# Optimization experiments

Measured on AMD Instinct MI355X. Metric: run time of the kernel, lower is better.

Reference implementation:

```python
import jax, jax.numpy as jnp
import numpy as np

B, D, L, G, K, U, OUT = 131072, 256, 3, 4, 128, 64, 10


def setup_inputs() -> dict:
    key = jax.random.key(0)
    k1, k2, k3, k4 = jax.random.split(key, 4)
    x = jax.random.normal(k1, (B, D), dtype=jnp.float32)
    # per-level, per-group input node coords into the previous level's output
    idx = jax.random.randint(k2, (L, G, K), 0, D, dtype=jnp.int32)
    # per-group kernels [fan_in, units] and biases [units], stacked
    W = jax.random.normal(k3, (L, G, K, U), dtype=jnp.float32) * 0.1
    b = jnp.zeros((L, G, U), dtype=jnp.float32)
    W_out = jax.random.normal(k4, (D, OUT), dtype=jnp.float32) * 0.1
    b_out = jnp.zeros((OUT,), dtype=jnp.float32)
    return {"x": x, "idx": idx, "W": W, "b": b, "W_out": W_out, "b_out": b_out}


def reference(x, idx, W, b, W_out, b_out):
    # Each topological level: for every dependency-group g, gather K scalar
    # columns from the previous level (the per-node slice+concat in the
    # original), tiny matmul [B,K]@[K,U] + bias, tanh; level output is the
    # concat of group outputs -> [B, G*U]. Groups share shapes, so they are
    # batched over axis g with a single einsum per level.
    h = x
    n_levels = W.shape[0]
    for l in range(n_levels):  # small fixed loop over topology levels
        gathered = h[:, idx[l]]                                  # [B, G, K]
        z = jnp.einsum('bgk,gku->bgu', gathered, W[l]) + b[l]    # [B, G, U]
        h = jnp.tanh(z).reshape(z.shape[0], -1)                  # [B, G*U]
    # output level: single group fed by all previous nodes, linear out activation
    return h @ W_out + b_out                                      # [B, OUT]
```

## Files before the change

### kernel.cpp

```cpp
#include <hip/hip_runtime.h>

typedef unsigned short ushort_t;
typedef __attribute__((ext_vector_type(8))) short short8;
typedef __attribute__((ext_vector_type(4))) float floatx4;
typedef __attribute__((ext_vector_type(4))) unsigned short ushort4v;

#define DD 256
#define LL 3
#define GG 4
#define KK 128
#define UU 64
#define OUTN 10
#define HSTRIDE 264

__device__ __forceinline__ ushort_t f2bf(float f) {
  unsigned u = __builtin_bit_cast(unsigned, f);
  u = (u + 0x7FFFu + ((u >> 16) & 1u)) >> 16;
  return (ushort_t)u;
}

__device__ __forceinline__ float fast_tanh(float x) {
  float e = __builtin_amdgcn_exp2f(x * 2.885390081777927f);
  return __builtin_fmaf(-2.0f, __builtin_amdgcn_rcpf(e + 1.0f), 1.0f);
}

__global__ __launch_bounds__(256) void prep_kernel(
    const int* __restrict__ idx, const float* __restrict__ W,
    const float* __restrict__ Wout, ushort_t* __restrict__ AT,
    ushort_t* __restrict__ WoT) {
  int b = blockIdx.x;
  int t = threadIdx.x;
  if (b < LL * DD) {
    int l = b >> 8, n = b & 255, g = n >> 6, u = n & 63;
    __shared__ int sidx[KK];
    __shared__ float sw[KK];
    if (t < KK) {
      sidx[t] = idx[(l * GG + g) * KK + t];
      sw[t]   = W[((size_t)((l * GG + g) * KK + t)) * UU + u];
    }
    __syncthreads();
    float s = 0.f;
#pragma unroll 8
    for (int j = 0; j < KK; j++) s += (sidx[j] == t) ? sw[j] : 0.f;
    AT[(b << 8) | t] = f2bf(s);
  } else {
    int e2 = (b - LL * DD) * 256 + t;
    int n = e2 >> 8, k = e2 & 255;
    WoT[e2] = (n < OUTN) ? f2bf(Wout[k * OUTN + n]) : (ushort_t)0;
  }
}

__global__ __launch_bounds__(256) void fused_kernel(
    const float* __restrict__ x, const float* __restrict__ bias,
    const float* __restrict__ bout, const ushort_t* __restrict__ AT,
    const ushort_t* __restrict__ WoT, float* __restrict__ out) {
  __shared__ ushort_t hbuf[64 * HSTRIDE];

  const int tid  = threadIdx.x;
  const int wave = tid >> 6;
  const int lane = tid & 63;
  const int quad = lane >> 4;
  const int l16  = lane & 15;
  const long row0 = (long)blockIdx.x * 64;

  const float4* xv = (const float4*)(x + row0 * DD);
#pragma unroll
  for (int i = 0; i < 16; i++) {
    int f  = tid + i * 256;
    int r  = f >> 6;
    int c4 = f & 63;
    float4 v = xv[r * 64 + c4];
    ushort4v uv;
    uv.x = f2bf(v.x); uv.y = f2bf(v.y); uv.z = f2bf(v.z); uv.w = f2bf(v.w);
    *(ushort4v*)&hbuf[r * HSTRIDE + c4 * 4] = uv;
  }
  __syncthreads();

  const floatx4 zero = {0.f, 0.f, 0.f, 0.f};

#pragma unroll
  for (int l = 0; l < 3; l++) {
    const ushort_t* A = AT + l * (DD * DD);

    short8 wf[4][8];
#pragma unroll
    for (int nt = 0; nt < 4; nt++)
#pragma unroll
      for (int ks = 0; ks < 8; ks++)
        wf[nt][ks] = *(const short8*)&A[(wave * 64 + nt * 16 + l16) * 256 + ks * 32 + quad * 8];

    floatx4 acc[4][4];
#pragma unroll
    for (int mt = 0; mt < 4; mt++)
#pragma unroll
      for (int nt = 0; nt < 4; nt++) acc[mt][nt] = zero;

#pragma unroll
    for (int ks = 0; ks < 8; ks++) {
      const int kb = ks * 32 + quad * 8;
      short8 bf[4];
#pragma unroll
      for (int mt = 0; mt < 4; mt++)
        bf[mt] = *(const short8*)&hbuf[(mt * 16 + l16) * HSTRIDE + kb];
#pragma unroll
      for (int mt = 0; mt < 4; mt++)
#pragma unroll
        for (int nt = 0; nt < 4; nt++)
          acc[mt][nt] = __builtin_amdgcn_mfma_f32_16x16x32_bf16(wf[nt][ks], bf[mt], acc[mt][nt], 0, 0, 0);
    }
    __syncthreads();

#pragma unroll
    for (int nt = 0; nt < 4; nt++) {
      float4 bv = *(const float4*)&bias[(l * GG + wave) * UU + nt * 16 + quad * 4];
#pragma unroll
      for (int mt = 0; mt < 4; mt++) {
        ushort4v hv;
        hv.x = f2bf(fast_tanh(acc[mt][nt][0] + bv.x));
        hv.y = f2bf(fast_tanh(acc[mt][nt][1] + bv.y));
        hv.z = f2bf(fast_tanh(acc[mt][nt][2] + bv.z));
        hv.w = f2bf(fast_tanh(acc[mt][nt][3] + bv.w));
        *(ushort4v*)&hbuf[(mt * 16 + l16) * HSTRIDE + wave * 64 + nt * 16 + quad * 4] = hv;
      }
    }
    __syncthreads();
  }

  short8 wof[8];
#pragma unroll
  for (int ks = 0; ks < 8; ks++)
    wof[ks] = *(const short8*)&WoT[l16 * 256 + ks * 32 + quad * 8];

  floatx4 accf = zero;
#pragma unroll
  for (int ks = 0; ks < 8; ks++) {
    short8 bf = *(const short8*)&hbuf[(wave * 16 + l16) * HSTRIDE + ks * 32 + quad * 8];
    accf = __builtin_amdgcn_mfma_f32_16x16x32_bf16(wof[ks], bf, accf, 0, 0, 0);
  }

  const long obase = (row0 + wave * 16 + l16) * OUTN;
  if (quad < 2) {
    float2 p0 = {accf[0] + bout[quad * 4 + 0], accf[1] + bout[quad * 4 + 1]};
    float2 p1 = {accf[2] + bout[quad * 4 + 2], accf[3] + bout[quad * 4 + 3]};
    *(float2*)&out[obase + quad * 4]     = p0;
    *(float2*)&out[obase + quad * 4 + 2] = p1;
  } else if (quad == 2) {
    float2 p0 = {accf[0] + bout[8], accf[1] + bout[9]};
    *(float2*)&out[obase + 8] = p0;
  }
}

extern "C" void kernel_launch(void* const* d_in, const int* in_sizes, int n_in,
                              void* d_out, int out_size, void* d_ws, size_t ws_size,
                              hipStream_t stream) {
  const float* x    = (const float*)d_in[0];
  const int*   idx  = (const int*)d_in[1];
  const float* W    = (const float*)d_in[2];
  const float* b    = (const float*)d_in[3];
  const float* Wout = (const float*)d_in[4];
  const float* bout = (const float*)d_in[5];
  float* out = (float*)d_out;

  ushort_t* AT  = (ushort_t*)d_ws;
  ushort_t* WoT = AT + LL * DD * DD;

  prep_kernel<<<LL * DD + 16, 256, 0, stream>>>(idx, W, Wout, AT, WoT);
  fused_kernel<<<2048, 256, 0, stream>>>(x, b, bout, AT, WoT, out);
}
```

Before: 298.0 us.

## Software-pipeline weight and activation fragment loads across levels and k-steps

Restructures the per-level MFMA loop so weight fragments are streamed two k-steps ahead and LDS activation fragments one k-step ahead, instead of loading all 32 weight fragments up front. The first two k-slices of the next level's weights (or the output weights) are prefetched before the barrier of the current level, and the first level's prefetch is issued before the x staging. Launch bounds now request two blocks per SM to cap register use. The goal is to hide global and LDS latency behind MFMA work, at the cost of more live registers and a possible spill under the new occupancy cap.

Result: faster. 286.5 us (-3.9%).

```diff
diff --git a/kernel.cpp b/kernel.cpp
--- a/kernel.cpp
+++ b/kernel.cpp
@@ -50,7 +50,67 @@
   }
 }
 
-__global__ __launch_bounds__(256) void fused_kernel(
+#define RUN_LEVEL(Ab, PF, BPTR)                                                \
+  {                                                                            \
+    const ushort_t* hsrc = hbuf + l16 * HSTRIDE + quad * 8;                    \
+    short8 wf[8][4];                                                           \
+    _Pragma("unroll") for (int nt = 0; nt < 4; nt++) {                         \
+      wf[0][nt] = pw0[nt];                                                     \
+      wf[1][nt] = pw1[nt];                                                     \
+    }                                                                          \
+    short8 bf[8][4];                                                           \
+    _Pragma("unroll") for (int mt = 0; mt < 4; mt++)                           \
+      bf[0][mt] = *(const short8*)&hsrc[mt * 16 * HSTRIDE];                    \
+    floatx4 acc[4][4];                                                         \
+    _Pragma("unroll") for (int mt = 0; mt < 4; mt++)                           \
+      _Pragma("unroll") for (int nt = 0; nt < 4; nt++) acc[mt][nt] = zero;     \
+    _Pragma("unroll") for (int ks = 0; ks < 8; ks++) {                         \
+      if (ks + 2 < 8) {                                                        \
+        _Pragma("unroll") for (int nt = 0; nt < 4; nt++)                       \
+          wf[ks + 2][nt] = *(const short8*)&(Ab)[nt * 4096 + (ks + 2) * 32];   \
+      }                                                                        \
+      if (ks + 1 < 8) {                                                        \
+        _Pragma("unroll") for (int mt = 0; mt < 4; mt++)                       \
+          bf[ks + 1][mt] =                                                     \
+              *(const short8*)&hsrc[mt * 16 * HSTRIDE + (ks + 1) * 32];        \
+      }                                                                        \
+      _Pragma("unroll") for (int mt = 0; mt < 4; mt++)                         \
+        _Pragma("unroll") for (int nt = 0; nt < 4; nt++)                       \
+          acc[mt][nt] = __builtin_amdgcn_mfma_f32_16x16x32_bf16(               \
+              wf[ks][nt], bf[ks][mt], acc[mt][nt], 0, 0, 0);                   \
+    }                                                                          \
+    PF;                                                                        \
+    __syncthreads();                 \
+    _Pragma("unroll") for (int nt = 0; nt < 4; nt++) {                         \
+      float4 bv = *(const float4*)&(BPTR)[nt * 16 + quad * 4];                 \
+      _Pragma("unroll") for (int mt = 0; mt < 4; mt++) {                       \
+        ushort4v hv;                                                           \
+        hv.x = f2bf(fast_tanh(acc[mt][nt][0] + bv.x));                         \
+        hv.y = f2bf(fast_tanh(acc[mt][nt][1] + bv.y));                         \
+        hv.z = f2bf(fast_tanh(acc[mt][nt][2] + bv.z));                         \
+        hv.w = f2bf(fast_tanh(acc[mt][nt][3] + bv.w));                         \
+        *(ushort4v*)&hbuf[(mt * 16 + l16) * HSTRIDE + wave * 64 + nt * 16 +    \
+                          quad * 4] = hv;                                      \
+      }                                                                        \
+    }                                                                          \
+    __syncthreads();                                                           \
+  }
+
+#define PF_NEXT(Anext)                                                         \
+  {                                                                            \
+    _Pragma("unroll") for (int nt = 0; nt < 4; nt++)                           \
+        pw0[nt] = *(const short8*)&(Anext)[nt * 4096];                         \
+    _Pragma("unroll") for (int nt = 0; nt < 4; nt++)                           \
+        pw1[nt] = *(const short8*)&(Anext)[nt * 4096 + 32];                    \
+  }
+
+#define PF_WOUT                                                                \
+  {                                                                            \
+    _Pragma("unroll") for (int ks = 0; ks < 8; ks++)                           \
+        wof[ks] = *(const short8*)&WoT[l16 * 256 + ks * 32 + quad * 8];        \
+  }
+
+__global__ __launch_bounds__(256, 2) void fused_kernel(
     const float* __restrict__ x, const float* __restrict__ bias,
     const float* __restrict__ bout, const ushort_t* __restrict__ AT,
     const ushort_t* __restrict__ WoT, float* __restrict__ out) {
@@ -62,6 +122,14 @@
   const int quad = lane >> 4;
   const int l16  = lane & 15;
   const long row0 = (long)blockIdx.x * 64;
+  const floatx4 zero = {0.f, 0.f, 0.f, 0.f};
+
+  const ushort_t* A0 = AT + (wave * 64 + l16) * 256 + quad * 8;
+  const ushort_t* A1 = A0 + 65536;
+  const ushort_t* A2 = A0 + 131072;
+
+  short8 pw0[4], pw1[4], wof[8];
+  PF_NEXT(A0);
 
   const float4* xv = (const float4*)(x + row0 * DD);
 #pragma unroll
@@ -76,66 +144,19 @@
   }
   __syncthreads();
 
-  const floatx4 zero = {0.f, 0.f, 0.f, 0.f};
+  const float* b0 = bias + (0 * GG + wave) * UU;
+  const float* b1 = bias + (1 * GG + wave) * UU;
+  const float* b2 = bias + (2 * GG + wave) * UU;
 
-#pragma unroll
-  for (int l = 0; l < 3; l++) {
-    const ushort_t* A = AT + l * (DD * DD);
-
-    short8 wf[4][8];
-#pragma unroll
-    for (int nt = 0; nt < 4; nt++)
-#pragma unroll
-      for (int ks = 0; ks < 8; ks++)
-        wf[nt][ks] = *(const short8*)&A[(wave * 64 + nt * 16 + l16) * 256 + ks * 32 + quad * 8];
-
-    floatx4 acc[4][4];
-#pragma unroll
-    for (int mt = 0; mt < 4; mt++)
-#pragma unroll
-      for (int nt = 0; nt < 4; nt++) acc[mt][nt] = zero;
-
-#pragma unroll
-    for (int ks = 0; ks < 8; ks++) {
-      const int kb = ks * 32 + quad * 8;
-      short8 bf[4];
-#pragma unroll
-      for (int mt = 0; mt < 4; mt++)
-        bf[mt] = *(const short8*)&hbuf[(mt * 16 + l16) * HSTRIDE + kb];
-#pragma unroll
-      for (int mt = 0; mt < 4; mt++)
-#pragma unroll
-        for (int nt = 0; nt < 4; nt++)
-          acc[mt][nt] = __builtin_amdgcn_mfma_f32_16x16x32_bf16(wf[nt][ks], bf[mt], acc[mt][nt], 0, 0, 0);
-    }
-    __syncthreads();
-
-#pragma unroll
-    for (int nt = 0; nt < 4; nt++) {
-      float4 bv = *(const float4*)&bias[(l * GG + wave) * UU + nt * 16 + quad * 4];
-#pragma unroll
-      for (int mt = 0; mt < 4; mt++) {
-        ushort4v hv;
-        hv.x = f2bf(fast_tanh(acc[mt][nt][0] + bv.x));
-        hv.y = f2bf(fast_tanh(acc[mt][nt][1] + bv.y));
-        hv.z = f2bf(fast_tanh(acc[mt][nt][2] + bv.z));
-        hv.w = f2bf(fast_tanh(acc[mt][nt][3] + bv.w));
-        *(ushort4v*)&hbuf[(mt * 16 + l16) * HSTRIDE + wave * 64 + nt * 16 + quad * 4] = hv;
-      }
-    }
-    __syncthreads();
-  }
-
-  short8 wof[8];
-#pragma unroll
-  for (int ks = 0; ks < 8; ks++)
-    wof[ks] = *(const short8*)&WoT[l16 * 256 + ks * 32 + quad * 8];
+  RUN_LEVEL(A0, PF_NEXT(A1), b0);
+  RUN_LEVEL(A1, PF_NEXT(A2), b1);
+  RUN_LEVEL(A2, PF_WOUT,     b2);
 
   floatx4 accf = zero;
 #pragma unroll
   for (int ks = 0; ks < 8; ks++) {
-    short8 bf = *(const short8*)&hbuf[(wave * 16 + l16) * HSTRIDE + ks * 32 + quad * 8];
-    accf = __builtin_amdgcn_mfma_f32_16x16x32_bf16(wof[ks], bf, accf, 0, 0, 0);
+    short8 bfr = *(const short8*)&hbuf[(wave * 16 + l16) * HSTRIDE + ks * 32 + quad * 8];
+    accf = __builtin_amdgcn_mfma_f32_16x16x32_bf16(wof[ks], bfr, accf, 0, 0, 0);
   }
 
   const long obase = (row0 + wave * 16 + l16) * OUTN;
```

## Double rows per block and stream weight fragments with prefetch per k-step

Applied to the files above, without the earlier changes.

Each block now handles 128 rows instead of 64, so every weight fragment loaded from global memory is reused across twice as many MFMA tiles. Instead of preloading all 32 weight fragments per level, the kernel streams them one k-step ahead (double-buffered) to reduce register pressure. The bias is folded into the accumulator initialisation, and bf16 packing uses a perm-based round-half-up instead of round-to-nearest-even. The output stores are widened to float4. The larger shared buffer and launch_bounds(256,2) lower occupancy, trading latency hiding for reuse.

Result: faster. 271.1 us (-9.0%).

```diff
diff --git a/kernel.cpp b/kernel.cpp
--- a/kernel.cpp
+++ b/kernel.cpp
@@ -3,7 +3,6 @@
 typedef unsigned short ushort_t;
 typedef __attribute__((ext_vector_type(8))) short short8;
 typedef __attribute__((ext_vector_type(4))) float floatx4;
-typedef __attribute__((ext_vector_type(4))) unsigned short ushort4v;
 
 #define DD 256
 #define LL 3
@@ -12,11 +11,18 @@
 #define UU 64
 #define OUTN 10
 #define HSTRIDE 264
+#define MROWS 128
 
 __device__ __forceinline__ ushort_t f2bf(float f) {
   unsigned u = __builtin_bit_cast(unsigned, f);
   u = (u + 0x7FFFu + ((u >> 16) & 1u)) >> 16;
   return (ushort_t)u;
+}
+
+__device__ __forceinline__ unsigned pack_bf2(float lo, float hi) {
+  unsigned a = __builtin_bit_cast(unsigned, hi) + 0x8000u;
+  unsigned b = __builtin_bit_cast(unsigned, lo) + 0x8000u;
+  return __builtin_amdgcn_perm(a, b, 0x07060302u);
 }
 
 __device__ __forceinline__ float fast_tanh(float x) {
@@ -50,77 +56,80 @@
   }
 }
 
-__global__ __launch_bounds__(256) void fused_kernel(
+__global__ __launch_bounds__(256, 2) void fused_kernel(
     const float* __restrict__ x, const float* __restrict__ bias,
     const float* __restrict__ bout, const ushort_t* __restrict__ AT,
     const ushort_t* __restrict__ WoT, float* __restrict__ out) {
-  __shared__ ushort_t hbuf[64 * HSTRIDE];
+  __shared__ ushort_t hbuf[MROWS * HSTRIDE];
 
   const int tid  = threadIdx.x;
   const int wave = tid >> 6;
   const int lane = tid & 63;
   const int quad = lane >> 4;
   const int l16  = lane & 15;
-  const long row0 = (long)blockIdx.x * 64;
+  const long row0 = (long)blockIdx.x * MROWS;
 
   const float4* xv = (const float4*)(x + row0 * DD);
 #pragma unroll
-  for (int i = 0; i < 16; i++) {
+  for (int i = 0; i < 32; i++) {
     int f  = tid + i * 256;
     int r  = f >> 6;
     int c4 = f & 63;
     float4 v = xv[r * 64 + c4];
-    ushort4v uv;
-    uv.x = f2bf(v.x); uv.y = f2bf(v.y); uv.z = f2bf(v.z); uv.w = f2bf(v.w);
-    *(ushort4v*)&hbuf[r * HSTRIDE + c4 * 4] = uv;
+    uint2 w;
+    w.x = pack_bf2(v.x, v.y);
+    w.y = pack_bf2(v.z, v.w);
+    *(uint2*)&hbuf[r * HSTRIDE + c4 * 4] = w;
   }
   __syncthreads();
 
-  const floatx4 zero = {0.f, 0.f, 0.f, 0.f};
+#pragma unroll 1
+  for (int l = 0; l < 3; l++) {
+    const ushort_t* Ab = AT + l * (DD * DD) + (wave * UU + l16) * DD + quad * 8;
+    const ushort_t* hsrc = hbuf + l16 * HSTRIDE + quad * 8;
 
+    floatx4 acc[8][4];
 #pragma unroll
-  for (int l = 0; l < 3; l++) {
-    const ushort_t* A = AT + l * (DD * DD);
+    for (int nt = 0; nt < 4; nt++) {
+      float4 bv = *(const float4*)&bias[(l * GG + wave) * UU + nt * 16 + quad * 4];
+      floatx4 ini = {bv.x, bv.y, bv.z, bv.w};
+#pragma unroll
+      for (int mt = 0; mt < 8; mt++) acc[mt][nt] = ini;
+    }
 
-    short8 wf[4][8];
+    short8 wf[4], wfn[4];
 #pragma unroll
-    for (int nt = 0; nt < 4; nt++)
-#pragma unroll
-      for (int ks = 0; ks < 8; ks++)
-        wf[nt][ks] = *(const short8*)&A[(wave * 64 + nt * 16 + l16) * 256 + ks * 32 + quad * 8];
-
-    floatx4 acc[4][4];
-#pragma unroll
-    for (int mt = 0; mt < 4; mt++)
-#pragma unroll
-      for (int nt = 0; nt < 4; nt++) acc[mt][nt] = zero;
+    for (int nt = 0; nt < 4; nt++) wf[nt] = *(const short8*)&Ab[nt * 16 * DD];
 
 #pragma unroll
     for (int ks = 0; ks < 8; ks++) {
-      const int kb = ks * 32 + quad * 8;
-      short8 bf[4];
-#pragma unroll
-      for (int mt = 0; mt < 4; mt++)
-        bf[mt] = *(const short8*)&hbuf[(mt * 16 + l16) * HSTRIDE + kb];
-#pragma unroll
-      for (int mt = 0; mt < 4; mt++)
+      if (ks < 7) {
 #pragma unroll
         for (int nt = 0; nt < 4; nt++)
-          acc[mt][nt] = __builtin_amdgcn_mfma_f32_16x16x32_bf16(wf[nt][ks], bf[mt], acc[mt][nt], 0, 0, 0);
+          wfn[nt] = *(const short8*)&Ab[nt * 16 * DD + (ks + 1) * 32];
+      }
+      short8 bf[8];
+#pragma unroll
+      for (int mt = 0; mt < 8; mt++)
+        bf[mt] = *(const short8*)&hsrc[mt * 16 * HSTRIDE + ks * 32];
+#pragma unroll
+      for (int mt = 0; mt < 8; mt++)
+#pragma unroll
+        for (int nt = 0; nt < 4; nt++)
+          acc[mt][nt] = __builtin_amdgcn_mfma_f32_16x16x32_bf16(wf[nt], bf[mt], acc[mt][nt], 0, 0, 0);
+#pragma unroll
+      for (int nt = 0; nt < 4; nt++) wf[nt] = wfn[nt];
     }
     __syncthreads();
 
 #pragma unroll
     for (int nt = 0; nt < 4; nt++) {
-      float4 bv = *(const float4*)&bias[(l * GG + wave) * UU + nt * 16 + quad * 4];
 #pragma unroll
-      for (int mt = 0; mt < 4; mt++) {
-        ushort4v hv;
-        hv.x = f2bf(fast_tanh(acc[mt][nt][0] + bv.x));
-        hv.y = f2bf(fast_tanh(acc[mt][nt][1] + bv.y));
-        hv.z = f2bf(fast_tanh(acc[mt][nt][2] + bv.z));
-        hv.w = f2bf(fast_tanh(acc[mt][nt][3] + bv.w));
-        *(ushort4v*)&hbuf[(mt * 16 + l16) * HSTRIDE + wave * 64 + nt * 16 + quad * 4] = hv;
+      for (int mt = 0; mt < 8; mt++) {
+        uint2 w;
+        w.x = pack_bf2(fast_tanh(acc[mt][nt][0]), fast_tanh(acc[mt][nt][1]));
+        w.y = pack_bf2(fast_tanh(acc[mt][nt][2]), fast_tanh(acc[mt][nt][3]));
+        *(uint2*)&hbuf[(mt * 16 + l16) * HSTRIDE + wave * UU + nt * 16 + quad * 4] = w;
       }
     }
     __syncthreads();
@@ -129,24 +138,26 @@
   short8 wof[8];
 #pragma unroll
   for (int ks = 0; ks < 8; ks++)
-    wof[ks] = *(const short8*)&WoT[l16 * 256 + ks * 32 + quad * 8];
+    wof[ks] = *(const short8*)&WoT[l16 * DD + ks * 32 + quad * 8];
 
-  floatx4 accf = zero;
+  const floatx4 zero = {0.f, 0.f, 0.f, 0.f};
 #pragma unroll
-  for (int ks = 0; ks < 8; ks++) {
-    short8 bf = *(const short8*)&hbuf[(wave * 16 + l16) * HSTRIDE + ks * 32 + quad * 8];
-    accf = __builtin_amdgcn_mfma_f32_16x16x32_bf16(wof[ks], bf, accf, 0, 0, 0);
-  }
-
-  const long obase = (row0 + wave * 16 + l16) * OUTN;
-  if (quad < 2) {
-    float2 p0 = {accf[0] + bout[quad * 4 + 0], accf[1] + bout[quad * 4 + 1]};
-    float2 p1 = {accf[2] + bout[quad * 4 + 2], accf[3] + bout[quad * 4 + 3]};
-    *(float2*)&out[obase + quad * 4]     = p0;
-    *(float2*)&out[obase + quad * 4 + 2] = p1;
-  } else if (quad == 2) {
-    float2 p0 = {accf[0] + bout[8], accf[1] + bout[9]};
-    *(float2*)&out[obase + 8] = p0;
+  for (int s = 0; s < 2; s++) {
+    floatx4 accf = zero;
+#pragma unroll
+    for (int ks = 0; ks < 8; ks++) {
+      short8 bfr = *(const short8*)&hbuf[(wave * 32 + s * 16 + l16) * HSTRIDE + ks * 32 + quad * 8];
+      accf = __builtin_amdgcn_mfma_f32_16x16x32_bf16(wof[ks], bfr, accf, 0, 0, 0);
+    }
+    const long obase = (row0 + wave * 32 + s * 16 + l16) * OUTN;
+    if (quad < 2) {
+      float4 p = {accf[0] + bout[quad * 4 + 0], accf[1] + bout[quad * 4 + 1],
+                  accf[2] + bout[quad * 4 + 2], accf[3] + bout[quad * 4 + 3]};
+      *(float4*)&out[obase + quad * 4] = p;
+    } else if (quad == 2) {
+      float2 p = {accf[0] + bout[8], accf[1] + bout[9]};
+      *(float2*)&out[obase + 8] = p;
+    }
   }
 }
 
@@ -165,5 +176,5 @@
   ushort_t* WoT = AT + LL * DD * DD;
 
   prep_kernel<<<LL * DD + 16, 256, 0, stream>>>(idx, W, Wout, AT, WoT);
-  fused_kernel<<<2048, 256, 0, stream>>>(x, b, bout, AT, WoT, out);
+  fused_kernel<<<131072 / MROWS, 256, 0, stream>>>(x, b, bout, AT, WoT, out);
 }
```
